# Optimization experiments

Hardware: AMD Instinct MI355X
Metric: run time of the kernel (lower is better)

## Reference

```python
import jax, jax.numpy as jnp
from jax import lax
import numpy as np

K = 4          # kernel_size
DEPTH = 2      # sig_depth
B, S, CIN = 64, 1024, 5
H1, H2 = 64, 16
OUT = 32
C1 = H2 + CIN + 1            # channels entering signature1 (include_original + include_time)
SIG_C1 = C1 + C1 * C1        # 506
SIG_C2 = H2 + H2 * H2        # 272


def setup_inputs() -> dict:
    key = jax.random.key(0)
    ks = jax.random.split(key, 12)
    def w(k, shape, fan_in):
        return jax.random.normal(k, shape, jnp.float32) * (1.0 / np.sqrt(fan_in))
    inp = {}
    inp["x"] = jax.random.normal(ks[0], (B, S, CIN), jnp.float32)
    inp["lengths"] = jax.random.randint(ks[1], (B,), S // 2, S + 1)
    # Augment 1: Conv1d(CIN->H1, k=K), Conv1d(H1->H1, 1), Conv1d(H1->H2, 1)
    inp["a1_w0"] = w(ks[2], (H1, CIN, K), CIN * K); inp["a1_b0"] = jnp.zeros((H1,), jnp.float32)
    inp["a1_w1"] = w(ks[3], (H1, H1, 1), H1);       inp["a1_b1"] = jnp.zeros((H1,), jnp.float32)
    inp["a1_w2"] = w(ks[4], (H2, H1, 1), H1);       inp["a1_b2"] = jnp.zeros((H2,), jnp.float32)
    # Augment 2: Conv1d(SIG_C1->H1, k=K), Conv1d(H1->H1, 1), Conv1d(H1->H2, 1)
    inp["a2_w0"] = w(ks[5], (H1, SIG_C1, K), SIG_C1 * K); inp["a2_b0"] = jnp.zeros((H1,), jnp.float32)
    inp["a2_w1"] = w(ks[6], (H1, H1, 1), H1);             inp["a2_b1"] = jnp.zeros((H1,), jnp.float32)
    inp["a2_w2"] = w(ks[7], (H2, H1, 1), H1);             inp["a2_b2"] = jnp.zeros((H2,), jnp.float32)
    inp["lin_w"] = w(ks[8], (OUT, SIG_C2), SIG_C2)
    inp["lin_b"] = jnp.zeros((OUT,), jnp.float32)
    return inp


def _conv1d(x, w, b):
    # x: (B, C, L), w: (O, I, k) -> (B, O, L-k+1), VALID (no padding), stride 1
    y = lax.conv_general_dilated(x, w, (1,), 'VALID', dimension_numbers=('NCH', 'OIH', 'NCH'))
    return y + b[None, :, None]


def _augment(x, ws, bs, kernel_size, include_original, include_time):
    # signatory.Augment: relu between convs, none after last; concat [original_trunc, time, conv_out]
    b_, s_, _ = x.shape
    L = s_ - kernel_size + 1
    pieces = []
    if include_original:
        pieces.append(x[:, kernel_size - 1:, :])
    if include_time:
        t = jnp.linspace(0.0, 1.0, L, dtype=x.dtype)
        pieces.append(jnp.broadcast_to(t[None, :, None], (b_, L, 1)))
    h = jnp.swapaxes(x, 1, 2)
    h = _conv1d(h, ws[0], bs[0])
    for wi, bi in zip(ws[1:], bs[1:]):
        h = _conv1d(jax.nn.relu(h), wi, bi)
    pieces.append(jnp.swapaxes(h, 1, 2))
    return jnp.concatenate(pieces, axis=2)


def _sig_exp(dx, depth):
    # tensor-algebra exp of a linear segment: level k = dx^{\otimes k} / k!
    levels = [dx]
    cur = dx
    for k in range(2, depth + 1):
        cur = (cur[..., :, None] * dx[..., None, :]).reshape(dx.shape[:-1] + (-1,)) / k
        levels.append(cur)
    return levels


def _chen(a, b, depth):
    # Chen's relation: (a*b)_k = a_k + sum_{i=1}^{k-1} a_i (x) b_{k-i} + b_k
    out = []
    for k in range(1, depth + 1):
        acc = a[k - 1] + b[k - 1]
        for i in range(1, k):
            acc = acc + (a[i - 1][:, :, None] * b[k - i - 1][:, None, :]).reshape(acc.shape)
        out.append(acc)
    return tuple(out)


def _signature(x, depth, stream):
    # basepoint=True: prepend zero point, so increments are diff with zero prepended
    b_, s_, c_ = x.shape
    dx = jnp.diff(x, axis=1, prepend=jnp.zeros((b_, 1, c_), x.dtype))
    exps = tuple(jnp.moveaxis(e, 1, 0) for e in _sig_exp(dx, depth))  # each (S, B, c^k)
    init = tuple(jnp.zeros((b_, c_ ** k), x.dtype) for k in range(1, depth + 1))  # identity (levels=0)
    def step(carry, e):
        new = _chen(carry, e, depth)
        return new, (new if stream else None)
    carry, ys = lax.scan(step, init, exps)
    if stream:
        return jnp.concatenate([jnp.moveaxis(y, 0, 1) for y in ys], axis=2)
    return jnp.concatenate(carry, axis=1)


def _become_constant(x, lengths):
    # y[i,j] = x[i,j] if j < lengths[i] else x[i, lengths[i]-1]
    b_, s_, _ = x.shape
    idx = jnp.minimum(jnp.arange(s_)[None, :], (lengths - 1)[:, None])
    return x[jnp.arange(b_)[:, None], idx]


def reference(x, lengths, a1_w0, a1_b0, a1_w1, a1_b1, a1_w2, a1_b2,
              a2_w0, a2_b0, a2_w1, a2_b1, a2_w2, a2_b2, lin_w, lin_b):
    h = _augment(x, (a1_w0, a1_w1, a1_w2), (a1_b0, a1_b1, a1_b2), K, True, True)   # (B, S-K+1, C1)
    s1 = _signature(h, DEPTH, True)                                                # (B, S-K+1, SIG_C1)
    h2 = _augment(s1, (a2_w0, a2_w1, a2_w2), (a2_b0, a2_b1, a2_b2), K, False, False)  # (B, S-2K+2, H2)
    adj = lengths - 2 * K + 2
    h2 = _become_constant(h2, adj)
    s2 = _signature(h2, DEPTH, False)                                              # (B, SIG_C2)
    return s2 @ lin_w.T + lin_b
```

## Files before the change

### kernel.cpp

```cpp
#include <hip/hip_runtime.h>
#include <hip/hip_bf16.h>

#define B_    64
#define S_    1024
#define CIN   5
#define K_    4
#define H1    64
#define H2    16
#define OUT_  32
#define L1_   1021
#define C1    22
#define C1SQ  484
#define SIGC1 506
#define L2_   1018
#define SIGC2 272
#define NCH   32
#define CH1   32

typedef __attribute__((ext_vector_type(8))) short short8;
typedef __attribute__((ext_vector_type(16))) float f32x16;

__device__ __forceinline__ unsigned short f2bf(float v) {
  __hip_bfloat16 h = __float2bfloat16(v);
  return *reinterpret_cast<unsigned short*>(&h);
}
__device__ __forceinline__ float bf2f(unsigned short u) {
  __hip_bfloat16 h;
  *reinterpret_cast<unsigned short*>(&h) = u;
  return __bfloat162float(h);
}

__global__ __launch_bounds__(256) void aug1_kernel(
    const float* __restrict__ x,
    const float* __restrict__ w0, const float* __restrict__ b0,
    const float* __restrict__ w1, const float* __restrict__ b1,
    const float* __restrict__ w2, const float* __restrict__ b2,
    float* __restrict__ h) {
  int b = blockIdx.y;
  int l = blockIdx.x * 256 + threadIdx.x;
  if (l >= L1_) return;
  const float* xb = x + (size_t)b * S_ * CIN;

  float t1[H1];
#pragma unroll
  for (int o = 0; o < H1; ++o) t1[o] = b0[o];
  for (int j = 0; j < K_; ++j) {
    for (int c = 0; c < CIN; ++c) {
      float xv = xb[(l + j) * CIN + c];
#pragma unroll
      for (int o = 0; o < H1; ++o) t1[o] += xv * w0[o * (CIN * K_) + c * K_ + j];
    }
  }
#pragma unroll
  for (int o = 0; o < H1; ++o) t1[o] = fmaxf(t1[o], 0.f);

  float t3[H2];
#pragma unroll
  for (int q = 0; q < H2; ++q) t3[q] = b2[q];
  for (int ch = 0; ch < 4; ++ch) {
    float t2c[16];
    for (int oc = 0; oc < 16; ++oc) {
      int o = ch * 16 + oc;
      float a = b1[o];
#pragma unroll
      for (int i = 0; i < H1; ++i) a += t1[i] * w1[o * H1 + i];
      t2c[oc] = fmaxf(a, 0.f);
    }
#pragma unroll
    for (int q = 0; q < H2; ++q) {
      float a = t3[q];
#pragma unroll
      for (int oc = 0; oc < 16; ++oc) a += t2c[oc] * w2[q * H1 + ch * 16 + oc];
      t3[q] = a;
    }
  }

  float* hr = h + ((size_t)b * L1_ + l) * C1;
#pragma unroll
  for (int c = 0; c < CIN; ++c) hr[c] = xb[(l + K_ - 1) * CIN + c];
  hr[CIN] = (float)l / (float)(L1_ - 1);
#pragma unroll
  for (int q = 0; q < H2; ++q) hr[CIN + 1 + q] = t3[q];
}

__global__ __launch_bounds__(512) void sig1a_kernel(const float* __restrict__ h, float* __restrict__ tot1) {
  int kt = blockIdx.x, b = blockIdx.y;
  int tid = threadIdx.x;
  if (tid >= C1SQ) return;
  int start = kt * 128;
  const float* hb = h + (size_t)b * L1_ * C1;
  int i = tid / C1, j = tid - i * C1;
  float hpi = 0.f, hpj = 0.f;
  if (kt > 0) {
    hpi = hb[(start - 1) * C1 + i];
    hpj = hb[(start - 1) * C1 + j];
  }
  float pi = 0.f, pj = 0.f, s2 = 0.f;
#pragma unroll 4
  for (int t = start; t < start + 128; ++t) {
    float ci = hb[t * C1 + i] - hpi;
    float cj = hb[t * C1 + j] - hpj;
    float dj = cj - pj;
    s2 += pi * dj + 0.5f * (ci - pi) * dj;
    pi = ci;
    pj = cj;
  }
  tot1[((size_t)b * 8 + kt) * C1SQ + tid] = s2;
}

__global__ __launch_bounds__(256) void wt2_kernel(const float* __restrict__ w0,
                                                  unsigned short* __restrict__ bhi,
                                                  unsigned short* __restrict__ blo) {
  int idx = blockIdx.x * 256 + threadIdx.x;
  if (idx >= 2 * 128 * 64 * 8) return;
  int e = idx & 7;
  int lane = (idx >> 3) & 63;
  int ksg = (idx >> 9) & 127;
  int ot = idx >> 16;
  int j = ksg >> 5, cc = (ksg >> 2) & 7, ks = ksg & 3;
  int o = ot * 32 + (lane & 31);
  int c = cc * 64 + ks * 16 + (lane >> 5) * 8 + e;
  float v = (c < SIGC1) ? w0[o * (SIGC1 * K_) + c * K_ + j] : 0.f;
  unsigned short hb16 = f2bf(v);
  bhi[idx] = hb16;
  blo[idx] = f2bf(v - bf2f(hb16));
}

__global__ __launch_bounds__(512) void conv2pw_kernel(
    const float* __restrict__ h, const float* __restrict__ tot1,
    const unsigned short* __restrict__ bpkhi, const unsigned short* __restrict__ bpklo,
    const float* __restrict__ b0,
    const float* __restrict__ w1, const float* __restrict__ b1,
    const float* __restrict__ w2, const float* __restrict__ b2,
    float* __restrict__ h2) {
  __shared__ __align__(16) char smem[151552];
  int tid = threadIdx.x;
  int lane = tid & 63, w = tid >> 6;
  int wm = w >> 1, wo = w & 1;
  int k = blockIdx.x, b = blockIdx.y, l0 = k * 128;
  const float* hb = h + (size_t)b * L1_ * C1;
  const char* bhg = (const char*)bpkhi;
  const char* blg = (const char*)bpklo;
  float* hs = (float*)smem;
  char* Abuf = smem + 12288;
  char* Bs = smem + 81920;
  float* gsum = (float*)(smem + 147456);
  float* s2pl = (float*)(smem + 149504);

  for (int idx = tid; idx < 137 * C1; idx += 512) {
    int r = idx / C1, c = idx - r * C1;
    float v = 0.f;
    if (!(k == 0 && r == 0)) {
      int hr = l0 - 1 + r;
      if (hr > L1_ - 1) hr = L1_ - 1;
      v = hb[hr * C1 + c];
    }
    hs[idx] = v;
  }
  if (tid < C1SQ) {
    int i = tid / C1, j = tid - i * C1;
    float s2pv = 0.f;
    for (int kp = 0; kp < k; ++kp) {
      float bvi = 0.f, bvj = 0.f;
      if (kp > 0) {
        bvi = hb[(128 * kp - 1) * C1 + i];
        bvj = hb[(128 * kp - 1) * C1 + j];
      }
      float bv1j = hb[(128 * (kp + 1) - 1) * C1 + j];
      s2pv += bvi * (bv1j - bvj) + tot1[((size_t)b * 8 + kp) * C1SQ + tid];
    }
    s2pl[tid] = s2pv;
  }
  __syncthreads();

  f32x16 aHH = {}, aHL = {}, aLH = {};
  int khalf = lane >> 5;
  int r0 = 32 * wm + (lane & 31);

  for (int cc = 0; cc < 8; ++cc) {
    if (cc) __syncthreads();
    for (int s = w; s < 64; s += 8) {
      int p = s >> 2, ot = (s >> 1) & 1, plane = s & 1;
      int jj = p >> 2, ks = p & 3;
      int ksg = jj * 32 + cc * 4 + ks;
      const char* src = (plane ? blg : bhg) + (size_t)(ot * 128 + ksg) * 1024 + lane * 16;
      __builtin_amdgcn_global_load_lds(
          (const __attribute__((address_space(1))) void*)src,
          (__attribute__((address_space(3))) void*)(Bs + ((p * 2 + ot) * 2 + plane) * 1024), 16, 0, 0);
    }
    char* Ah = Abuf + (cc & 1) * 34816;
    char* Al = Ah + 17408;
    int c = cc * 64 + lane;
    bool isS2 = (c >= C1 && c < SIGC1);
    int ii = 0, jj2 = 0;
    if (isS2) {
      int idx = c - C1;
      ii = idx / C1;
      jj2 = idx - ii * C1;
    }
    float hpi = hs[ii], hpj = hs[jj2];
    int u0 = w * 17;
    {
      float pi = hs[u0 * C1 + ii] - hpi;
      float pj = hs[u0 * C1 + jj2] - hpj;
      float loc = 0.f;
      for (int s = 0; s < 17; ++s) {
        int u = u0 + s;
        float ci = hs[(u + 1) * C1 + ii] - hpi;
        float cj = hs[(u + 1) * C1 + jj2] - hpj;
        float dj = cj - pj;
        loc += pi * dj + 0.5f * (ci - pi) * dj;
        pi = ci;
        pj = cj;
      }
      gsum[w * 64 + lane] = loc;
    }
    __syncthreads();
    {
      float s2r = isS2 ? s2pl[c - C1] : 0.f;
      for (int gp = 0; gp < w; ++gp) s2r += gsum[gp * 64 + lane];
      float pi = hs[u0 * C1 + ii] - hpi;
      float pj = hs[u0 * C1 + jj2] - hpj;
      for (int s = 0; s < 17; ++s) {
        int u = u0 + s;
        float v;
        if (isS2) {
          float ci = hs[(u + 1) * C1 + ii] - hpi;
          float cj = hs[(u + 1) * C1 + jj2] - hpj;
          float dj = cj - pj;
          s2r += pi * dj + 0.5f * (ci - pi) * dj;
          pi = ci;
          pj = cj;
          v = s2r + hpi * cj;
        } else if (c < C1) {
          v = hs[(u + 1) * C1 + c];
        } else {
          v = 0.f;
        }
        unsigned short hb16 = f2bf(v);
        unsigned short lb16 = f2bf(v - bf2f(hb16));
        int boff = u * 128 + (((lane >> 3) ^ (u & 7)) << 4) + (lane & 7) * 2;
        *(unsigned short*)(Ah + boff) = hb16;
        *(unsigned short*)(Al + boff) = lb16;
      }
    }
    __syncthreads();
#pragma unroll
    for (int j = 0; j < 4; ++j) {
      int ra = r0 + j;
      int rx = ra & 7;
      const char* ab = Ah + ra * 128;
      const char* abl = Al + ra * 128;
#pragma unroll
      for (int ks = 0; ks < 4; ++ks) {
        int p = j * 4 + ks;
        const char* bb = Bs + (size_t)((p * 2 + wo) * 2) * 1024 + lane * 16;
        short8 b_h = *(const short8*)bb;
        short8 b_l = *(const short8*)(bb + 1024);
        int g0 = ((ks * 2 + khalf) ^ rx) << 4;
        short8 vh = *(const short8*)(ab + g0);
        short8 vl = *(const short8*)(abl + g0);
        aHH = __builtin_amdgcn_mfma_f32_32x32x16_bf16(vh, b_h, aHH, 0, 0, 0);
        aHL = __builtin_amdgcn_mfma_f32_32x32x16_bf16(vh, b_l, aHL, 0, 0, 0);
        aLH = __builtin_amdgcn_mfma_f32_32x32x16_bf16(vl, b_h, aLH, 0, 0, 0);
      }
    }
  }
  __syncthreads();
  float* t1s = (float*)smem;
  float* t2s = (float*)(smem + 33280);
  float* wl = (float*)(smem + 66560);
  for (int i2 = tid; i2 < 4096; i2 += 512) wl[i2] = w1[i2];
  for (int i2 = tid; i2 < 1024; i2 += 512) wl[4096 + i2] = w2[i2];
  {
    int col = 32 * wo + (lane & 31);
    float bbv = b0[col];
    int rbase = 32 * wm + 4 * khalf;
#pragma unroll
    for (int rg = 0; rg < 16; ++rg) {
      int row = (rg & 3) + 8 * (rg >> 2) + rbase;
      t1s[row * 65 + col] = fmaxf(aHH[rg] + aHL[rg] + aLH[rg] + bbv, 0.f);
    }
  }
  __syncthreads();
  {
    int row = tid >> 2, q = tid & 3;
    const float* trow = t1s + row * 65;
    float tr[64];
#pragma unroll
    for (int i2 = 0; i2 < 64; ++i2) tr[i2] = trow[i2];
#pragma unroll
    for (int oc = 0; oc < 16; ++oc) {
      int o = q * 16 + oc;
      float a = b1[o];
      const float4* wr = (const float4*)(wl + o * 64);
#pragma unroll
      for (int i4 = 0; i4 < 16; ++i4) {
        float4 wv = wr[i4];
        a += tr[i4 * 4] * wv.x + tr[i4 * 4 + 1] * wv.y +
             tr[i4 * 4 + 2] * wv.z + tr[i4 * 4 + 3] * wv.w;
      }
      t2s[row * 65 + o] = fmaxf(a, 0.f);
    }
  }
  __syncthreads();
  {
    int row = tid >> 2, pg = tid & 3;
    int l = l0 + row;
    if (l < L2_) {
      const float* trow = t2s + row * 65;
      float tr2[64];
#pragma unroll
      for (int i2 = 0; i2 < 64; ++i2) tr2[i2] = trow[i2];
      float* outr = h2 + ((size_t)b * L2_ + l) * H2;
#pragma unroll
      for (int pp = 0; pp < 4; ++pp) {
        int pch = pg * 4 + pp;
        float a = b2[pch];
        const float4* wr = (const float4*)(wl + 4096 + pch * 64);
#pragma unroll
        for (int i4 = 0; i4 < 16; ++i4) {
          float4 wv = wr[i4];
          a += tr2[i4 * 4] * wv.x + tr2[i4 * 4 + 1] * wv.y +
               tr2[i4 * 4 + 2] * wv.z + tr2[i4 * 4 + 3] * wv.w;
        }
        outr[pch] = a;
      }
    }
  }
}

__global__ __launch_bounds__(256) void sig2a_kernel(const float* __restrict__ h2, const int* __restrict__ lengths,
                                                    float* __restrict__ s2tot2) {
  int k = blockIdx.x, b = blockIdx.y;
  int tid = threadIdx.x;
  int i = tid >> 4, j = tid & 15;
  int adjm1 = lengths[b] - (2 * K_ - 2) - 1;
  int start = k * CH1, end = min(start + CH1 - 1, L2_ - 1);
  size_t oidx = ((size_t)b * NCH + k) * 256 + tid;
  if (k > 0 && start - 1 >= adjm1) {
    s2tot2[oidx] = 0.f;
    return;
  }
  const float* h2b = h2 + (size_t)b * L2_ * H2;
  float hpi = 0.f, hpj = 0.f;
  if (k > 0) {
    int row = min(start - 1, adjm1);
    hpi = h2b[row * H2 + i];
    hpj = h2b[row * H2 + j];
  }
  float pi = 0.f, pj = 0.f, s2 = 0.f;
#pragma unroll 4
  for (int t = start; t <= end; ++t) {
    int row = min(t, adjm1);
    float ci = h2b[row * H2 + i] - hpi;
    float cj = h2b[row * H2 + j] - hpj;
    float dj = cj - pj;
    s2 += pi * dj + 0.5f * (ci - pi) * dj;
    pi = ci;
    pj = cj;
  }
  s2tot2[oidx] = s2;
}

__global__ __launch_bounds__(256) void sig2b_kernel(const float* __restrict__ h2, const int* __restrict__ lengths,
                                                    const float* __restrict__ s2tot2,
                                                    const float* __restrict__ lin_w, const float* __restrict__ lin_b,
                                                    float* __restrict__ out) {
  int b = blockIdx.x;
  int tid = threadIdx.x;
  int i = tid >> 4, j = tid & 15;
  int adjm1 = lengths[b] - (2 * K_ - 2) - 1;
  const float* h2b = h2 + (size_t)b * L2_ * H2;
  __shared__ float bv[NCH + 1][H2];
  __shared__ float s2s[SIGC2];
  for (int idx = tid; idx < (NCH + 1) * H2; idx += 256) {
    int kk = idx >> 4, c = idx & 15;
    float v = 0.f;
    if (kk > 0) {
      int row = min(min(CH1 * kk - 1, L2_ - 1), adjm1);
      v = h2b[row * H2 + c];
    }
    bv[kk][c] = v;
  }
  __syncthreads();
  float s2 = 0.f;
  for (int k = 0; k < NCH; ++k) {
    s2 += bv[k][i] * (bv[k + 1][j] - bv[k][j]) + s2tot2[((size_t)b * NCH + k) * 256 + tid];
  }
  s2s[H2 + tid] = s2;
  if (tid < H2) s2s[tid] = bv[NCH][tid];
  __syncthreads();
  if (tid < OUT_) {
    float a = lin_b[tid];
    for (int c = 0; c < SIGC2; ++c) a += s2s[c] * lin_w[tid * SIGC2 + c];
    out[b * OUT_ + tid] = a;
  }
}

extern "C" void kernel_launch(void* const* d_in, const int* in_sizes, int n_in,
                              void* d_out, int out_size, void* d_ws, size_t ws_size,
                              hipStream_t stream) {
  const float* x      = (const float*)d_in[0];
  const int*   lengths= (const int*)d_in[1];
  const float* a1_w0  = (const float*)d_in[2];
  const float* a1_b0  = (const float*)d_in[3];
  const float* a1_w1  = (const float*)d_in[4];
  const float* a1_b1  = (const float*)d_in[5];
  const float* a1_w2  = (const float*)d_in[6];
  const float* a1_b2  = (const float*)d_in[7];
  const float* a2_w0  = (const float*)d_in[8];
  const float* a2_b0  = (const float*)d_in[9];
  const float* a2_w1  = (const float*)d_in[10];
  const float* a2_b1  = (const float*)d_in[11];
  const float* a2_w2  = (const float*)d_in[12];
  const float* a2_b2  = (const float*)d_in[13];
  const float* lin_w  = (const float*)d_in[14];
  const float* lin_b  = (const float*)d_in[15];
  float* outp = (float*)d_out;

  float* ws = (float*)d_ws;
  float* h = ws;
  unsigned short* bpkhi = (unsigned short*)(ws + 1437568);
  unsigned short* bpklo = bpkhi + 131072;
  float* h2 = ws + 1568640;
  float* tot1 = ws + 2611072;
  float* s2tot2 = ws + 2858880;

  aug1_kernel<<<dim3(4, B_), 256, 0, stream>>>(x, a1_w0, a1_b0, a1_w1, a1_b1, a1_w2, a1_b2, h);
  wt2_kernel<<<(2 * 128 * 64 * 8 + 255) / 256, 256, 0, stream>>>(a2_w0, bpkhi, bpklo);
  sig1a_kernel<<<dim3(7, B_), 512, 0, stream>>>(h, tot1);
  conv2pw_kernel<<<dim3(8, B_), 512, 0, stream>>>(h, tot1, bpkhi, bpklo, a2_b0,
                                                  a2_w1, a2_b1, a2_w2, a2_b2, h2);
  sig2a_kernel<<<dim3(NCH, B_), 256, 0, stream>>>(h2, lengths, s2tot2);
  sig2b_kernel<<<B_, 256, 0, stream>>>(h2, lengths, s2tot2, lin_w, lin_b, outp);
}
```

Measured before the change: 290.2 us.

## Shrink conv2 LDS footprint with 32-channel chunks and merge weight-pack with sig1a

The conv2pw kernel now processes 32 signature channels per chunk over 16 iterations instead of 64 over 8. It drops the double-buffered A tile and the LDS copy of w1/w2, which cuts shared memory from about 148KB to 65KB so more blocks can be resident per CU. The A tile layout changes to a column-slab format without XOR swizzling, and the scan is split into 16 groups of 9 rows. The wt2 weight-packing kernel is merged into the sig1a kernel as extra blocks, saving one launch. The cost is twice as many barriers and B loads per block, pointwise weights read from global/cache, and possible LDS bank conflicts from the unswizzled layout.

After: 410.8 us. 41.5% more time.

```diff
diff --git a/kernel.cpp b/kernel.cpp
--- a/kernel.cpp
+++ b/kernel.cpp
@@ -83,10 +83,29 @@
   for (int q = 0; q < H2; ++q) hr[CIN + 1 + q] = t3[q];
 }
 
-__global__ __launch_bounds__(512) void sig1a_kernel(const float* __restrict__ h, float* __restrict__ tot1) {
-  int kt = blockIdx.x, b = blockIdx.y;
+__global__ __launch_bounds__(512) void wtsig_kernel(
+    const float* __restrict__ h, float* __restrict__ tot1,
+    const float* __restrict__ a2w0,
+    unsigned short* __restrict__ bhi, unsigned short* __restrict__ blo) {
+  int blk = blockIdx.x;
   int tid = threadIdx.x;
+  if (blk >= 448) {
+    int idx = (blk - 448) * 512 + tid;
+    int e = idx & 7;
+    int lane = (idx >> 3) & 63;
+    int ksg = (idx >> 9) & 127;
+    int ot = idx >> 16;
+    int j = ksg >> 5, cc = (ksg >> 2) & 7, ks = ksg & 3;
+    int o = ot * 32 + (lane & 31);
+    int c = cc * 64 + ks * 16 + (lane >> 5) * 8 + e;
+    float v = (c < SIGC1) ? a2w0[o * (SIGC1 * K_) + c * K_ + j] : 0.f;
+    unsigned short hb16 = f2bf(v);
+    bhi[idx] = hb16;
+    blo[idx] = f2bf(v - bf2f(hb16));
+    return;
+  }
   if (tid >= C1SQ) return;
+  int kt = blk / 64, b = blk - kt * 64;
   int start = kt * 128;
   const float* hb = h + (size_t)b * L1_ * C1;
   int i = tid / C1, j = tid - i * C1;
@@ -108,24 +127,6 @@
   tot1[((size_t)b * 8 + kt) * C1SQ + tid] = s2;
 }
 
-__global__ __launch_bounds__(256) void wt2_kernel(const float* __restrict__ w0,
-                                                  unsigned short* __restrict__ bhi,
-                                                  unsigned short* __restrict__ blo) {
-  int idx = blockIdx.x * 256 + threadIdx.x;
-  if (idx >= 2 * 128 * 64 * 8) return;
-  int e = idx & 7;
-  int lane = (idx >> 3) & 63;
-  int ksg = (idx >> 9) & 127;
-  int ot = idx >> 16;
-  int j = ksg >> 5, cc = (ksg >> 2) & 7, ks = ksg & 3;
-  int o = ot * 32 + (lane & 31);
-  int c = cc * 64 + ks * 16 + (lane >> 5) * 8 + e;
-  float v = (c < SIGC1) ? w0[o * (SIGC1 * K_) + c * K_ + j] : 0.f;
-  unsigned short hb16 = f2bf(v);
-  bhi[idx] = hb16;
-  blo[idx] = f2bf(v - bf2f(hb16));
-}
-
 __global__ __launch_bounds__(512) void conv2pw_kernel(
     const float* __restrict__ h, const float* __restrict__ tot1,
     const unsigned short* __restrict__ bpkhi, const unsigned short* __restrict__ bpklo,
@@ -133,7 +134,7 @@
     const float* __restrict__ w1, const float* __restrict__ b1,
     const float* __restrict__ w2, const float* __restrict__ b2,
     float* __restrict__ h2) {
-  __shared__ __align__(16) char smem[151552];
+  __shared__ __align__(16) char smem[66560];
   int tid = threadIdx.x;
   int lane = tid & 63, w = tid >> 6;
   int wm = w >> 1, wo = w & 1;
@@ -142,10 +143,11 @@
   const char* bhg = (const char*)bpkhi;
   const char* blg = (const char*)bpklo;
   float* hs = (float*)smem;
-  char* Abuf = smem + 12288;
-  char* Bs = smem + 81920;
-  float* gsum = (float*)(smem + 147456);
-  float* s2pl = (float*)(smem + 149504);
+  char* Ah = smem + 12064;
+  char* Al = smem + 20896;
+  char* Bs = smem + 29728;
+  float* gsum = (float*)(smem + 62496);
+  float* s2pl = (float*)(smem + 64544);
 
   for (int idx = tid; idx < 137 * C1; idx += 512) {
     int r = idx / C1, c = idx - r * C1;
@@ -176,21 +178,20 @@
   f32x16 aHH = {}, aHL = {}, aLH = {};
   int khalf = lane >> 5;
   int r0 = 32 * wm + (lane & 31);
-
-  for (int cc = 0; cc < 8; ++cc) {
+  int cl = tid & 31;
+  int g = tid >> 5;
+
+  for (int cc = 0; cc < 16; ++cc) {
     if (cc) __syncthreads();
-    for (int s = w; s < 64; s += 8) {
-      int p = s >> 2, ot = (s >> 1) & 1, plane = s & 1;
-      int jj = p >> 2, ks = p & 3;
-      int ksg = jj * 32 + cc * 4 + ks;
+    for (int s = w; s < 32; s += 8) {
+      int pair = s >> 2, ot = (s >> 1) & 1, plane = s & 1;
+      int ksg = (pair >> 1) * 32 + cc * 2 + (pair & 1);
       const char* src = (plane ? blg : bhg) + (size_t)(ot * 128 + ksg) * 1024 + lane * 16;
       __builtin_amdgcn_global_load_lds(
           (const __attribute__((address_space(1))) void*)src,
-          (__attribute__((address_space(3))) void*)(Bs + ((p * 2 + ot) * 2 + plane) * 1024), 16, 0, 0);
-    }
-    char* Ah = Abuf + (cc & 1) * 34816;
-    char* Al = Ah + 17408;
-    int c = cc * 64 + lane;
+          (__attribute__((address_space(3))) void*)(Bs + ((pair * 2 + ot) * 2 + plane) * 1024), 16, 0, 0);
+    }
+    int c = cc * 32 + cl;
     bool isS2 = (c >= C1 && c < SIGC1);
     int ii = 0, jj2 = 0;
     if (isS2) {
@@ -199,67 +200,71 @@
       jj2 = idx - ii * C1;
     }
     float hpi = hs[ii], hpj = hs[jj2];
-    int u0 = w * 17;
+    int u0 = g * 9;
     {
       float pi = hs[u0 * C1 + ii] - hpi;
       float pj = hs[u0 * C1 + jj2] - hpj;
       float loc = 0.f;
-      for (int s = 0; s < 17; ++s) {
+#pragma unroll
+      for (int s = 0; s < 9; ++s) {
         int u = u0 + s;
-        float ci = hs[(u + 1) * C1 + ii] - hpi;
-        float cj = hs[(u + 1) * C1 + jj2] - hpj;
-        float dj = cj - pj;
-        loc += pi * dj + 0.5f * (ci - pi) * dj;
-        pi = ci;
-        pj = cj;
-      }
-      gsum[w * 64 + lane] = loc;
+        if (u < 136) {
+          float ci = hs[(u + 1) * C1 + ii] - hpi;
+          float cj = hs[(u + 1) * C1 + jj2] - hpj;
+          float dj = cj - pj;
+          loc += pi * dj + 0.5f * (ci - pi) * dj;
+          pi = ci;
+          pj = cj;
+        }
+      }
+      gsum[g * 32 + cl] = loc;
     }
     __syncthreads();
     {
       float s2r = isS2 ? s2pl[c - C1] : 0.f;
-      for (int gp = 0; gp < w; ++gp) s2r += gsum[gp * 64 + lane];
+      for (int gp = 0; gp < g; ++gp) s2r += gsum[gp * 32 + cl];
       float pi = hs[u0 * C1 + ii] - hpi;
       float pj = hs[u0 * C1 + jj2] - hpj;
-      for (int s = 0; s < 17; ++s) {
+      int slot = (cl >> 3) * 2208 + (cl & 7) * 2;
+#pragma unroll
+      for (int s = 0; s < 9; ++s) {
         int u = u0 + s;
-        float v;
-        if (isS2) {
-          float ci = hs[(u + 1) * C1 + ii] - hpi;
-          float cj = hs[(u + 1) * C1 + jj2] - hpj;
-          float dj = cj - pj;
-          s2r += pi * dj + 0.5f * (ci - pi) * dj;
-          pi = ci;
-          pj = cj;
-          v = s2r + hpi * cj;
-        } else if (c < C1) {
-          v = hs[(u + 1) * C1 + c];
-        } else {
-          v = 0.f;
+        if (u < 136) {
+          float v;
+          if (isS2) {
+            float ci = hs[(u + 1) * C1 + ii] - hpi;
+            float cj = hs[(u + 1) * C1 + jj2] - hpj;
+            float dj = cj - pj;
+            s2r += pi * dj + 0.5f * (ci - pi) * dj;
+            pi = ci;
+            pj = cj;
+            v = s2r + hpi * cj;
+          } else if (c < C1) {
+            v = hs[(u + 1) * C1 + c];
+          } else {
+            v = 0.f;
+          }
+          unsigned short hb16 = f2bf(v);
+          unsigned short lb16 = f2bf(v - bf2f(hb16));
+          int boff = slot + u * 16;
+          *(unsigned short*)(Ah + boff) = hb16;
+          *(unsigned short*)(Al + boff) = lb16;
         }
-        unsigned short hb16 = f2bf(v);
-        unsigned short lb16 = f2bf(v - bf2f(hb16));
-        int boff = u * 128 + (((lane >> 3) ^ (u & 7)) << 4) + (lane & 7) * 2;
-        *(unsigned short*)(Ah + boff) = hb16;
-        *(unsigned short*)(Al + boff) = lb16;
       }
     }
     __syncthreads();
 #pragma unroll
     for (int j = 0; j < 4; ++j) {
       int ra = r0 + j;
-      int rx = ra & 7;
-      const char* ab = Ah + ra * 128;
-      const char* abl = Al + ra * 128;
-#pragma unroll
-      for (int ks = 0; ks < 4; ++ks) {
-        int p = j * 4 + ks;
-        const char* bb = Bs + (size_t)((p * 2 + wo) * 2) * 1024 + lane * 16;
+#pragma unroll
+      for (int ks2 = 0; ks2 < 2; ++ks2) {
+        int pair = j * 2 + ks2;
+        const char* bb = Bs + (size_t)((pair * 2 + wo) * 2) * 1024 + lane * 16;
         short8 b_h = *(const short8*)bb;
         short8 b_l = *(const short8*)(bb + 1024);
-        int g0 = ((ks * 2 + khalf) ^ rx) << 4;
-        short8 vh = *(const short8*)(ab + g0);
-        short8 vl = *(const short8*)(abl + g0);
+        int aoff = (ks2 * 2 + khalf) * 2208 + ra * 16;
+        short8 vh = *(const short8*)(Ah + aoff);
+        short8 vl = *(const short8*)(Al + aoff);
         aHH = __builtin_amdgcn_mfma_f32_32x32x16_bf16(vh, b_h, aHH, 0, 0, 0);
         aHL = __builtin_amdgcn_mfma_f32_32x32x16_bf16(vh, b_l, aHL, 0, 0, 0);
         aLH = __builtin_amdgcn_mfma_f32_32x32x16_bf16(vl, b_h, aLH, 0, 0, 0);
@@ -269,9 +274,6 @@
   __syncthreads();
   float* t1s = (float*)smem;
   float* t2s = (float*)(smem + 33280);
-  float* wl = (float*)(smem + 66560);
-  for (int i2 = tid; i2 < 4096; i2 += 512) wl[i2] = w1[i2];
-  for (int i2 = tid; i2 < 1024; i2 += 512) wl[4096 + i2] = w2[i2];
   {
     int col = 32 * wo + (lane & 31);
     float bbv = b0[col];
@@ -293,7 +295,7 @@
     for (int oc = 0; oc < 16; ++oc) {
       int o = q * 16 + oc;
       float a = b1[o];
-      const float4* wr = (const float4*)(wl + o * 64);
+      const float4* wr = (const float4*)(w1 + o * 64);
 #pragma unroll
       for (int i4 = 0; i4 < 16; ++i4) {
         float4 wv = wr[i4];
@@ -317,7 +319,7 @@
       for (int pp = 0; pp < 4; ++pp) {
         int pch = pg * 4 + pp;
         float a = b2[pch];
-        const float4* wr = (const float4*)(wl + 4096 + pch * 64);
+        const float4* wr = (const float4*)(w2 + pch * 64);
 #pragma unroll
         for (int i4 = 0; i4 < 16; ++i4) {
           float4 wv = wr[i4];
@@ -428,8 +430,7 @@
   float* s2tot2 = ws + 2858880;
 
   aug1_kernel<<<dim3(4, B_), 256, 0, stream>>>(x, a1_w0, a1_b0, a1_w1, a1_b1, a1_w2, a1_b2, h);
-  wt2_kernel<<<(2 * 128 * 64 * 8 + 255) / 256, 256, 0, stream>>>(a2_w0, bpkhi, bpklo);
-  sig1a_kernel<<<dim3(7, B_), 512, 0, stream>>>(h, tot1);
+  wtsig_kernel<<<704, 512, 0, stream>>>(h, tot1, a2_w0, bpkhi, bpklo);
   conv2pw_kernel<<<dim3(8, B_), 512, 0, stream>>>(h, tot1, bpkhi, bpklo, a2_b0,
                                                   a2_w1, a2_b1, a2_w2, a2_b2, h2);
   sig2a_kernel<<<dim3(NCH, B_), 256, 0, stream>>>(h2, lengths, s2tot2);
```
